# Kernel tuning notes

Hardware: AMD Instinct MI355X
Metric: run time of the kernel (lower is better)

Reference implementation:

```python
import jax, jax.numpy as jnp
import numpy as np

B, S, H = 32, 2048, 1024


def setup_inputs() -> dict:
    key = jax.random.key(0)
    k1, k2, k3, k4, k5 = jax.random.split(key, 5)
    # scale linear weights like torch default init (~U(-1/sqrt(fan_in),..)); normal*small is fine for a numeric baseline
    return {
        "hidden": jax.random.normal(k1, (B, H), dtype=jnp.float32),
        "encoder_outputs": jax.random.normal(k2, (B, S, H), dtype=jnp.float32),
        "attn_w": jax.random.normal(k3, (H, 2 * H), dtype=jnp.float32) * (1.0 / np.sqrt(2 * H)),
        "attn_b": jax.random.normal(k4, (H,), dtype=jnp.float32) * (1.0 / np.sqrt(2 * H)),
        "v_w": jax.random.normal(k5, (1, H), dtype=jnp.float32) * (1.0 / np.sqrt(H)),
    }


def reference(hidden, encoder_outputs, attn_w, attn_b, v_w):
    # hidden: [B,H]; encoder_outputs: [B,S,H]
    # torch: cat((hidden repeated over S, enc), dim=2) @ attn_w.T + attn_b
    # Split attn_w columns: first H cols act on hidden, last H cols on enc.
    # Avoids materializing the repeated/concatenated [B,S,2H] tensor.
    Hdim = hidden.shape[-1]
    Wh = attn_w[:, :Hdim]   # [H, H] applied to hidden
    We = attn_w[:, Hdim:]   # [H, H] applied to encoder outputs
    # [B,1,H] + [B,S,H] + [H] -> tanh -> [B,S,H]
    e = jnp.tanh((hidden @ Wh.T)[:, None, :] + jnp.einsum('bsh,kh->bsk', encoder_outputs, We) + attn_b)
    scores = jnp.einsum('bsh,h->bs', e, v_w[0])          # [B,S], v has no bias
    attn_weights = jax.nn.softmax(scores, axis=1)        # softmax over source positions (dim=1)
    context = jnp.einsum('bs,bsh->bh', attn_weights, encoder_outputs)  # [B,H]
    output = jnp.concatenate([context, hidden], axis=1)  # [B,2H]
    return output, attn_weights[..., None]               # match torch shapes: [B,2H], [B,S,1]
```

## Files before the change

kernel.cpp:

```cpp
#include <hip/hip_runtime.h>
#include <stdint.h>

#define BATCH 32
#define SEQ   2048
#define HDIM  1024

typedef short short8 __attribute__((ext_vector_type(8)));
typedef float f32x4 __attribute__((ext_vector_type(4)));

#define LDS_K 1032

__device__ __forceinline__ unsigned short f2b(float f) {
    unsigned u = __float_as_uint(f);
    u += 0x7FFFu + ((u >> 16) & 1u);
    return (unsigned short)(u >> 16);
}

__device__ __forceinline__ float fast_tanh(float x) {
    float ex = __expf(2.0f * x);
    return 1.0f - 2.0f / (ex + 1.0f);
}

__global__ __launch_bounds__(256) void prep_kernel(
    const float* __restrict__ hidden, const float* __restrict__ attn_w,
    const float* __restrict__ attn_b, unsigned short* __restrict__ we_bf,
    float* __restrict__ qb) {
    int k = blockIdx.x;
    int tid = threadIdx.x;

    {
        const float4* src = (const float4*)(attn_w + (size_t)k * 2048 + 1024);
        float4 v = src[tid];
        ushort4 o;
        o.x = f2b(v.x); o.y = f2b(v.y); o.z = f2b(v.z); o.w = f2b(v.w);
        ((ushort4*)(we_bf + (size_t)k * HDIM))[tid] = o;
    }

    float part[BATCH];
#pragma unroll
    for (int b = 0; b < BATCH; ++b) part[b] = 0.0f;
    const float* wrow = attn_w + (size_t)k * 2048;
    for (int h = tid; h < HDIM; h += 256) {
        float w = wrow[h];
#pragma unroll
        for (int b = 0; b < BATCH; ++b) part[b] += w * hidden[b * HDIM + h];
    }
    __shared__ float red[4][BATCH];
    int lane = tid & 63, wv = tid >> 6;
#pragma unroll
    for (int b = 0; b < BATCH; ++b) {
        float v = part[b];
        v += __shfl_xor(v, 1);  v += __shfl_xor(v, 2);  v += __shfl_xor(v, 4);
        v += __shfl_xor(v, 8);  v += __shfl_xor(v, 16); v += __shfl_xor(v, 32);
        if (lane == 0) red[wv][b] = v;
    }
    __syncthreads();
    if (tid < BATCH) {
        float v = red[0][tid] + red[1][tid] + red[2][tid] + red[3][tid] + attn_b[k];
        qb[(size_t)tid * HDIM + k] = v;
    }
}

__global__ __launch_bounds__(512, 2) void score_gemm_kernel(
    const float* __restrict__ enc, const unsigned short* __restrict__ we_bf,
    const float* __restrict__ qb, const float* __restrict__ v_w,
    float* __restrict__ scores) {
    extern __shared__ char smem[];
    unsigned short* Als = (unsigned short*)smem;
    float* qb_lds = (float*)(smem + 64 * LDS_K * 2);
    float* v_lds  = qb_lds + HDIM;
    float* red    = v_lds + HDIM;

    int tid = threadIdx.x;
    int b   = blockIdx.x >> 5;
    int s0  = (blockIdx.x & 31) * 64;
    const float* arow = enc + ((size_t)b * SEQ + s0) * HDIM;

    qb_lds[tid]        = qb[(size_t)b * HDIM + tid];
    v_lds[tid]         = v_w[tid];
    if (tid < 512) {
        qb_lds[tid + 512] = qb[(size_t)b * HDIM + tid + 512];
        v_lds[tid + 512]  = v_w[tid + 512];
    }

#pragma unroll
    for (int it = 0; it < 16; ++it) {
        int c   = it * 512 + tid;
        int row = c >> 7;
        int c8  = c & 127;
        const float4* g = (const float4*)(arow + (size_t)row * HDIM + c8 * 8);
        float4 x = g[0], y = g[1];
        short8 o;
        o[0] = (short)f2b(x.x); o[1] = (short)f2b(x.y);
        o[2] = (short)f2b(x.z); o[3] = (short)f2b(x.w);
        o[4] = (short)f2b(y.x); o[5] = (short)f2b(y.y);
        o[6] = (short)f2b(y.z); o[7] = (short)f2b(y.w);
        *(short8*)(Als + row * LDS_K + c8 * 8) = o;
    }
    __syncthreads();

    int lane = tid & 63;
    int w    = tid >> 6;
    int l15  = lane & 15, q = lane >> 4;

    const unsigned short* bbase = we_bf + ((size_t)(w * 128 + l15)) * HDIM + q * 8;
    const unsigned short* albase = Als + l15 * LDS_K + q * 8;

    float sc[4][4];
#pragma unroll
    for (int mt = 0; mt < 4; ++mt)
#pragma unroll
        for (int r = 0; r < 4; ++r) sc[mt][r] = 0.0f;

    for (int g = 0; g < 2; ++g) {
        f32x4 acc[4][4];
#pragma unroll
        for (int mt = 0; mt < 4; ++mt)
#pragma unroll
            for (int nt = 0; nt < 4; ++nt) acc[mt][nt] = (f32x4)0.0f;

        const unsigned short* bg = bbase + (size_t)g * 64 * HDIM;
        for (int ks = 0; ks < 32; ++ks) {
            int ko = ks * 32;
            short8 af[4], bf[4];
#pragma unroll
            for (int mt = 0; mt < 4; ++mt)
                af[mt] = *(const short8*)(albase + mt * 16 * LDS_K + ko);
#pragma unroll
            for (int nt = 0; nt < 4; ++nt)
                bf[nt] = *(const short8*)(bg + (size_t)nt * 16 * HDIM + ko);
#pragma unroll
            for (int mt = 0; mt < 4; ++mt)
#pragma unroll
                for (int nt = 0; nt < 4; ++nt)
                    acc[mt][nt] = __builtin_amdgcn_mfma_f32_16x16x32_bf16(
                        af[mt], bf[nt], acc[mt][nt], 0, 0, 0);
        }

#pragma unroll
        for (int nt = 0; nt < 4; ++nt) {
            int n = w * 128 + g * 64 + nt * 16 + l15;
            float qv = qb_lds[n], vv = v_lds[n];
#pragma unroll
            for (int mt = 0; mt < 4; ++mt)
#pragma unroll
                for (int r = 0; r < 4; ++r)
                    sc[mt][r] += vv * fast_tanh(acc[mt][nt][r] + qv);
        }
    }

#pragma unroll
    for (int mt = 0; mt < 4; ++mt)
#pragma unroll
        for (int r = 0; r < 4; ++r) {
            float v = sc[mt][r];
            v += __shfl_xor(v, 1); v += __shfl_xor(v, 2);
            v += __shfl_xor(v, 4); v += __shfl_xor(v, 8);
            sc[mt][r] = v;
        }
    if (l15 == 0) {
#pragma unroll
        for (int mt = 0; mt < 4; ++mt)
#pragma unroll
            for (int r = 0; r < 4; ++r)
                red[w * 64 + mt * 16 + q * 4 + r] = sc[mt][r];
    }
    __syncthreads();
    if (tid < 64) {
        float t = 0.0f;
#pragma unroll
        for (int w2 = 0; w2 < 8; ++w2) t += red[w2 * 64 + tid];
        scores[(size_t)b * SEQ + s0 + tid] = t;
    }
}

__global__ __launch_bounds__(256) void softmax_kernel(
    const float* __restrict__ scores, const float* __restrict__ hidden,
    float* out) {
    int b = blockIdx.x, tid = threadIdx.x;
    const float* srow = scores + (size_t)b * SEQ;
    __shared__ float redm[4];
    __shared__ float reds[4];
    int lane = tid & 63, wv = tid >> 6;

    float loc[8];
    float m = -1e30f;
#pragma unroll
    for (int i = 0; i < 8; ++i) {
        loc[i] = srow[tid + i * 256];
        m = fmaxf(m, loc[i]);
    }
#pragma unroll
    for (int d = 1; d < 64; d <<= 1) m = fmaxf(m, __shfl_xor(m, d));
    if (lane == 0) redm[wv] = m;
    __syncthreads();
    m = fmaxf(fmaxf(redm[0], redm[1]), fmaxf(redm[2], redm[3]));

    float sum = 0.0f;
#pragma unroll
    for (int i = 0; i < 8; ++i) {
        float e = __expf(loc[i] - m);
        loc[i] = e;
        sum += e;
    }
#pragma unroll
    for (int d = 1; d < 64; d <<= 1) sum += __shfl_xor(sum, d);
    if (lane == 0) reds[wv] = sum;
    __syncthreads();
    sum = reds[0] + reds[1] + reds[2] + reds[3];
    float inv = 1.0f / sum;

#pragma unroll
    for (int i = 0; i < 8; ++i)
        out[BATCH * SEQ + (size_t)b * SEQ + tid + i * 256] = loc[i] * inv;

    for (int i = tid; i < HDIM; i += 256) {
        out[(size_t)b * 2048 + i] = 0.0f;
        out[(size_t)b * 2048 + 1024 + i] = hidden[(size_t)b * HDIM + i];
    }
}

__global__ __launch_bounds__(256) void context_kernel(
    const float* __restrict__ enc, const float* weights_src, float* out) {
    int id = blockIdx.x;
    int sc = id & 7, hc = (id >> 3) & 3, b = id >> 5;
    int tid = threadIdx.x;
    __shared__ float wl[256];
    wl[tid] = weights_src[BATCH * SEQ + (size_t)b * SEQ + sc * 256 + tid];
    __syncthreads();
    const float* ebase = enc + ((size_t)b * SEQ + sc * 256) * HDIM + hc * 256 + tid;
    float acc = 0.0f;
#pragma unroll 4
    for (int s = 0; s < 256; ++s) acc += wl[s] * ebase[(size_t)s * HDIM];
    atomicAdd(&out[(size_t)b * 2048 + hc * 256 + tid], acc);
}

extern "C" void kernel_launch(void* const* d_in, const int* in_sizes, int n_in,
                              void* d_out, int out_size, void* d_ws, size_t ws_size,
                              hipStream_t stream) {
    const float* hidden = (const float*)d_in[0];
    const float* enc    = (const float*)d_in[1];
    const float* attn_w = (const float*)d_in[2];
    const float* attn_b = (const float*)d_in[3];
    const float* v_w    = (const float*)d_in[4];
    float* out = (float*)d_out;

    char* ws = (char*)d_ws;
    unsigned short* we_bf = (unsigned short*)ws;
    float* qb     = (float*)(ws + (size_t)2097152);
    float* scores = (float*)(ws + (size_t)2097152 + 131072);

    prep_kernel<<<1024, 256, 0, stream>>>(hidden, attn_w, attn_b, we_bf, qb);

    size_t smem = (size_t)64 * LDS_K * 2 + HDIM * 4 * 2 + 8 * 64 * 4;
    score_gemm_kernel<<<1024, 512, smem, stream>>>(enc, we_bf, qb, v_w, scores);

    softmax_kernel<<<32, 256, 0, stream>>>(scores, hidden, out);

    context_kernel<<<1024, 256, 0, stream>>>(enc, out, out);
}
```

Baseline: 662.2 us.

## Pre-convert encoder outputs to bf16 and retile score GEMM with LDS staging

Adds a kernel that converts the encoder outputs to bf16 once. The score GEMM is restructured into 128x128 output tiles, staging A and B through swizzled LDS with direct global-to-LDS loads, and partial scores are combined with atomics into a pre-zeroed buffer. The context reduction now reads the bf16 copy with vectorized loads. The aim is better MFMA utilization and reuse of the weight tile, at the cost of an extra full write/read pass over the encoder tensor and reduced precision in the context sum.

```diff
diff --git a/kernel.cpp b/kernel.cpp
--- a/kernel.cpp
+++ b/kernel.cpp
@@ -7,26 +7,47 @@
 
 typedef short short8 __attribute__((ext_vector_type(8)));
 typedef float f32x4 __attribute__((ext_vector_type(4)));
-
-#define LDS_K 1032
 
 __device__ __forceinline__ unsigned short f2b(float f) {
     unsigned u = __float_as_uint(f);
     u += 0x7FFFu + ((u >> 16) & 1u);
     return (unsigned short)(u >> 16);
 }
-
+__device__ __forceinline__ float b2f(unsigned short u) {
+    return __uint_as_float(((unsigned)u) << 16);
+}
 __device__ __forceinline__ float fast_tanh(float x) {
     float ex = __expf(2.0f * x);
     return 1.0f - 2.0f / (ex + 1.0f);
 }
 
+__device__ __forceinline__ void gl2lds16(const unsigned short* g, unsigned short* l) {
+    __builtin_amdgcn_global_load_lds(
+        (const __attribute__((address_space(1))) unsigned int*)g,
+        (__attribute__((address_space(3))) unsigned int*)l, 16, 0, 0);
+}
+
+__global__ __launch_bounds__(256) void enc_convert(
+    const float* __restrict__ enc, unsigned short* __restrict__ enc_bf) {
+    size_t i = ((size_t)blockIdx.x * 256 + threadIdx.x) * 8;
+    const float4* s = (const float4*)(enc + i);
+    float4 a = s[0], b = s[1];
+    short8 o;
+    o[0] = (short)f2b(a.x); o[1] = (short)f2b(a.y);
+    o[2] = (short)f2b(a.z); o[3] = (short)f2b(a.w);
+    o[4] = (short)f2b(b.x); o[5] = (short)f2b(b.y);
+    o[6] = (short)f2b(b.z); o[7] = (short)f2b(b.w);
+    *(short8*)(enc_bf + i) = o;
+}
+
 __global__ __launch_bounds__(256) void prep_kernel(
     const float* __restrict__ hidden, const float* __restrict__ attn_w,
     const float* __restrict__ attn_b, unsigned short* __restrict__ we_bf,
-    float* __restrict__ qb) {
+    float* __restrict__ qb, float* __restrict__ scores) {
     int k = blockIdx.x;
     int tid = threadIdx.x;
+
+    if (tid < 64) scores[(size_t)k * 64 + tid] = 0.0f;
 
     {
         const float4* src = (const float4*)(attn_w + (size_t)k * 2048 + 1024);
@@ -61,74 +82,62 @@
     }
 }
 
-__global__ __launch_bounds__(512, 2) void score_gemm_kernel(
-    const float* __restrict__ enc, const unsigned short* __restrict__ we_bf,
+__global__ __launch_bounds__(256) void score_gemm_kernel(
+    const unsigned short* __restrict__ enc_bf, const unsigned short* __restrict__ we_bf,
     const float* __restrict__ qb, const float* __restrict__ v_w,
     float* __restrict__ scores) {
-    extern __shared__ char smem[];
-    unsigned short* Als = (unsigned short*)smem;
-    float* qb_lds = (float*)(smem + 64 * LDS_K * 2);
-    float* v_lds  = qb_lds + HDIM;
-    float* red    = v_lds + HDIM;
-
-    int tid = threadIdx.x;
-    int b   = blockIdx.x >> 5;
-    int s0  = (blockIdx.x & 31) * 64;
-    const float* arow = enc + ((size_t)b * SEQ + s0) * HDIM;
-
-    qb_lds[tid]        = qb[(size_t)b * HDIM + tid];
-    v_lds[tid]         = v_w[tid];
-    if (tid < 512) {
-        qb_lds[tid + 512] = qb[(size_t)b * HDIM + tid + 512];
-        v_lds[tid + 512]  = v_w[tid + 512];
-    }
-
-#pragma unroll
-    for (int it = 0; it < 16; ++it) {
-        int c   = it * 512 + tid;
-        int row = c >> 7;
-        int c8  = c & 127;
-        const float4* g = (const float4*)(arow + (size_t)row * HDIM + c8 * 8);
-        float4 x = g[0], y = g[1];
-        short8 o;
-        o[0] = (short)f2b(x.x); o[1] = (short)f2b(x.y);
-        o[2] = (short)f2b(x.z); o[3] = (short)f2b(x.w);
-        o[4] = (short)f2b(y.x); o[5] = (short)f2b(y.y);
-        o[6] = (short)f2b(y.z); o[7] = (short)f2b(y.w);
-        *(short8*)(Als + row * LDS_K + c8 * 8) = o;
-    }
-    __syncthreads();
-
-    int lane = tid & 63;
-    int w    = tid >> 6;
-    int l15  = lane & 15, q = lane >> 4;
-
-    const unsigned short* bbase = we_bf + ((size_t)(w * 128 + l15)) * HDIM + q * 8;
-    const unsigned short* albase = Als + l15 * LDS_K + q * 8;
-
-    float sc[4][4];
+    __shared__ unsigned short Als[128 * 64];
+    __shared__ unsigned short Bls[128 * 64];
+
+    int tid  = threadIdx.x;
+    int lane = tid & 63, w = tid >> 6;
+    int wm = w & 1, wn = w >> 1;
+    int i15 = lane & 15, q = lane >> 4;
+
+    int ntile = blockIdx.x & 7;
+    int mtile = blockIdx.x >> 3;
+    int b  = mtile >> 4;
+    int s0 = (mtile & 15) * 128;
+
+    const unsigned short* Ag = enc_bf + ((size_t)(b * SEQ + s0)) * HDIM;
+    const unsigned short* Bg = we_bf + (size_t)ntile * 128 * HDIM;
+
+    int srow   = lane >> 3;
+    int schunk = (lane & 7) ^ srow;
+    const unsigned short* Ag_l = Ag + (size_t)srow * HDIM + schunk * 8;
+    const unsigned short* Bg_l = Bg + (size_t)srow * HDIM + schunk * 8;
+    unsigned short* Al_w = Als + (w * 4) * 512;
+    unsigned short* Bl_w = Bls + (w * 4) * 512;
+
+    f32x4 acc[4][4];
 #pragma unroll
     for (int mt = 0; mt < 4; ++mt)
 #pragma unroll
-        for (int r = 0; r < 4; ++r) sc[mt][r] = 0.0f;
-
-    for (int g = 0; g < 2; ++g) {
-        f32x4 acc[4][4];
-#pragma unroll
-        for (int mt = 0; mt < 4; ++mt)
-#pragma unroll
-            for (int nt = 0; nt < 4; ++nt) acc[mt][nt] = (f32x4)0.0f;
-
-        const unsigned short* bg = bbase + (size_t)g * 64 * HDIM;
-        for (int ks = 0; ks < 32; ++ks) {
-            int ko = ks * 32;
+        for (int nt = 0; nt < 4; ++nt) acc[mt][nt] = (f32x4)0.0f;
+
+    const unsigned short* Abase = Als + (wm * 64 + i15) * 64;
+    const unsigned short* Bbase = Bls + (wn * 64 + i15) * 64;
+
+    for (int ks = 0; ks < 16; ++ks) {
+        if (ks) __syncthreads();
+        int k0 = ks * 64;
+#pragma unroll
+        for (int j = 0; j < 4; ++j) {
+            size_t roff = (size_t)((w * 4 + j) * 8) * HDIM + k0;
+            gl2lds16(Ag_l + roff, Al_w + j * 512);
+            gl2lds16(Bg_l + roff, Bl_w + j * 512);
+        }
+        __syncthreads();
+#pragma unroll
+        for (int k2 = 0; k2 < 2; ++k2) {
+            int xr = ((k2 * 4 + q) ^ (i15 & 7)) * 8;
             short8 af[4], bf[4];
 #pragma unroll
             for (int mt = 0; mt < 4; ++mt)
-                af[mt] = *(const short8*)(albase + mt * 16 * LDS_K + ko);
+                af[mt] = *(const short8*)(Abase + mt * 16 * 64 + xr);
 #pragma unroll
             for (int nt = 0; nt < 4; ++nt)
-                bf[nt] = *(const short8*)(bg + (size_t)nt * 16 * HDIM + ko);
+                bf[nt] = *(const short8*)(Bbase + nt * 16 * 64 + xr);
 #pragma unroll
             for (int mt = 0; mt < 4; ++mt)
 #pragma unroll
@@ -136,19 +145,25 @@
                     acc[mt][nt] = __builtin_amdgcn_mfma_f32_16x16x32_bf16(
                         af[mt], bf[nt], acc[mt][nt], 0, 0, 0);
         }
-
-#pragma unroll
-        for (int nt = 0; nt < 4; ++nt) {
-            int n = w * 128 + g * 64 + nt * 16 + l15;
-            float qv = qb_lds[n], vv = v_lds[n];
-#pragma unroll
-            for (int mt = 0; mt < 4; ++mt)
-#pragma unroll
-                for (int r = 0; r < 4; ++r)
-                    sc[mt][r] += vv * fast_tanh(acc[mt][nt][r] + qv);
-        }
-    }
-
+    }
+
+    float sc[4][4];
+#pragma unroll
+    for (int mt = 0; mt < 4; ++mt)
+#pragma unroll
+        for (int r = 0; r < 4; ++r) sc[mt][r] = 0.0f;
+
+#pragma unroll
+    for (int nt = 0; nt < 4; ++nt) {
+        int n = ntile * 128 + wn * 64 + nt * 16 + i15;
+        float qv = qb[(size_t)b * HDIM + n];
+        float vv = v_w[n];
+#pragma unroll
+        for (int mt = 0; mt < 4; ++mt)
+#pragma unroll
+            for (int r = 0; r < 4; ++r)
+                sc[mt][r] += vv * fast_tanh(acc[mt][nt][r] + qv);
+    }
 #pragma unroll
     for (int mt = 0; mt < 4; ++mt)
 #pragma unroll
@@ -156,22 +171,9 @@
             float v = sc[mt][r];
             v += __shfl_xor(v, 1); v += __shfl_xor(v, 2);
             v += __shfl_xor(v, 4); v += __shfl_xor(v, 8);
-            sc[mt][r] = v;
+            if (i15 == 0)
+                atomicAdd(&scores[(size_t)b * SEQ + s0 + wm * 64 + mt * 16 + q * 4 + r], v);
         }
-    if (l15 == 0) {
-#pragma unroll
-        for (int mt = 0; mt < 4; ++mt)
-#pragma unroll
-            for (int r = 0; r < 4; ++r)
-                red[w * 64 + mt * 16 + q * 4 + r] = sc[mt][r];
-    }
-    __syncthreads();
-    if (tid < 64) {
-        float t = 0.0f;
-#pragma unroll
-        for (int w2 = 0; w2 < 8; ++w2) t += red[w2 * 64 + tid];
-        scores[(size_t)b * SEQ + s0 + tid] = t;
-    }
 }
 
 __global__ __launch_bounds__(256) void softmax_kernel(
@@ -221,18 +223,28 @@
 }
 
 __global__ __launch_bounds__(256) void context_kernel(
-    const float* __restrict__ enc, const float* weights_src, float* out) {
+    const unsigned short* __restrict__ enc_bf, const float* weights_src,
+    float* out) {
     int id = blockIdx.x;
-    int sc = id & 7, hc = (id >> 3) & 3, b = id >> 5;
+    int scid = id & 15, b = id >> 4;
     int tid = threadIdx.x;
-    __shared__ float wl[256];
-    wl[tid] = weights_src[BATCH * SEQ + (size_t)b * SEQ + sc * 256 + tid];
-    __syncthreads();
-    const float* ebase = enc + ((size_t)b * SEQ + sc * 256) * HDIM + hc * 256 + tid;
-    float acc = 0.0f;
+    __shared__ float wl[128];
+    if (tid < 128)
+        wl[tid] = weights_src[BATCH * SEQ + (size_t)b * SEQ + scid * 128 + tid];
+    __syncthreads();
+    const unsigned short* ebase =
+        enc_bf + ((size_t)(b * SEQ + scid * 128)) * HDIM + tid * 4;
+    float a0 = 0.f, a1 = 0.f, a2 = 0.f, a3 = 0.f;
 #pragma unroll 4
-    for (int s = 0; s < 256; ++s) acc += wl[s] * ebase[(size_t)s * HDIM];
-    atomicAdd(&out[(size_t)b * 2048 + hc * 256 + tid], acc);
+    for (int s = 0; s < 128; ++s) {
+        ushort4 u = *(const ushort4*)(ebase + (size_t)s * HDIM);
+        float w = wl[s];
+        a0 += w * b2f(u.x); a1 += w * b2f(u.y);
+        a2 += w * b2f(u.z); a3 += w * b2f(u.w);
+    }
+    float* o = out + (size_t)b * 2048 + tid * 4;
+    atomicAdd(o + 0, a0); atomicAdd(o + 1, a1);
+    atomicAdd(o + 2, a2); atomicAdd(o + 3, a3);
 }
 
 extern "C" void kernel_launch(void* const* d_in, const int* in_sizes, int n_in,
@@ -249,13 +261,11 @@
     unsigned short* we_bf = (unsigned short*)ws;
     float* qb     = (float*)(ws + (size_t)2097152);
     float* scores = (float*)(ws + (size_t)2097152 + 131072);
-
-    prep_kernel<<<1024, 256, 0, stream>>>(hidden, attn_w, attn_b, we_bf, qb);
-
-    size_t smem = (size_t)64 * LDS_K * 2 + HDIM * 4 * 2 + 8 * 64 * 4;
-    score_gemm_kernel<<<1024, 512, smem, stream>>>(enc, we_bf, qb, v_w, scores);
-
+    unsigned short* enc_bf = (unsigned short*)(ws + (size_t)2097152 + 131072 + 262144);
+
+    enc_convert<<<32768, 256, 0, stream>>>(enc, enc_bf);
+    prep_kernel<<<1024, 256, 0, stream>>>(hidden, attn_w, attn_b, we_bf, qb, scores);
+    score_gemm_kernel<<<4096, 256, 0, stream>>>(enc_bf, we_bf, qb, v_w, scores);
     softmax_kernel<<<32, 256, 0, stream>>>(scores, hidden, out);
-
-    context_kernel<<<1024, 256, 0, stream>>>(enc, out, out);
-}
+    context_kernel<<<512, 256, 0, stream>>>(enc_bf, out, out);
+}
```

Result: faster. 603.0 us (-8.9%).
